# Kernel tuning notes

Hardware: AMD Instinct MI355X
Metric: run time of the kernel (lower is better)

The kernel has to match this reference:

```python
import jax, jax.numpy as jnp
import numpy as np

N = 40000      # nodes
E = 640000     # edges (before self-loops)
F_IN = 32      # num_node_features
H = 8          # n_heads
C = 16         # hidden_channels
G = 1000       # graphs in batch
M = 256        # MLP_neurons
NEG_SLOPE = 0.2


def setup_inputs() -> dict:
    key = jax.random.key(0)
    ks = jax.random.split(key, 24)
    d = {}
    d["x"] = jax.random.normal(ks[0], (N, F_IN), jnp.float32)
    d["edge_index"] = jax.random.randint(ks[1], (2, E), 0, N, dtype=jnp.int32)
    d["batch"] = jnp.sort(jax.random.randint(ks[2], (N,), 0, G, dtype=jnp.int32))
    dims = [F_IN, H * C, H * C]
    k = 3
    for i in range(3):
        fin = dims[i]
        s = 1.0 / np.sqrt(fin)
        d[f"W{i}"] = jax.random.normal(ks[k], (fin, H * C), jnp.float32) * s; k += 1
        d[f"b{i}"] = jnp.zeros((H * C,), jnp.float32)
        d[f"as{i}"] = jax.random.normal(ks[k], (H, C), jnp.float32) * (1.0 / np.sqrt(C)); k += 1
        d[f"ad{i}"] = jax.random.normal(ks[k], (H, C), jnp.float32) * (1.0 / np.sqrt(C)); k += 1
    d["fW0"] = jax.random.normal(ks[k], (H * C, M), jnp.float32) * (1.0 / np.sqrt(H * C)); k += 1
    d["fb0"] = jnp.zeros((M,), jnp.float32)
    d["fW1"] = jax.random.normal(ks[k], (M, M), jnp.float32) * (1.0 / np.sqrt(M)); k += 1
    d["fb1"] = jnp.zeros((M,), jnp.float32)
    d["oW"] = jax.random.normal(ks[k], (M, 2), jnp.float32) * (1.0 / np.sqrt(M)); k += 1
    d["ob"] = jnp.zeros((2,), jnp.float32)
    return d


def _gat_layer(x, W, b, a_src, a_dst, src, dst):
    # x: [N, Fin] -> h: [N, H, C]
    h = (x @ W).reshape(N, H, C)
    al_src = jnp.einsum('nhc,hc->nh', h, a_src)   # [N, H]
    al_dst = jnp.einsum('nhc,hc->nh', h, a_dst)   # [N, H]
    # edge-wise attention logits (gather), LeakyReLU
    e = jax.nn.leaky_relu(al_src[src] + al_dst[dst], NEG_SLOPE)  # [E', H]
    # softmax over incoming edges of each dst node
    emax = jax.ops.segment_max(e, dst, num_segments=N)           # [N, H]
    ex = jnp.exp(e - emax[dst])
    denom = jax.ops.segment_sum(ex, dst, num_segments=N)         # [N, H]
    alpha = ex / denom[dst]
    # weighted scatter-aggregation of source features
    out = jax.ops.segment_sum(alpha[:, :, None] * h[src], dst, num_segments=N)  # [N, H, C]
    return out.reshape(N, H * C) + b


def reference(x, edge_index, batch, W0, b0, as0, ad0, W1, b1, as1, ad1,
              W2, b2, as2, ad2, fW0, fb0, fW1, fb1, oW, ob):
    # PyG GATConv adds self-loops by default
    loops = jnp.arange(N, dtype=edge_index.dtype)
    src = jnp.concatenate([edge_index[0], loops])
    dst = jnp.concatenate([edge_index[1], loops])
    h = x
    for (W, b, a_s, a_d) in ((W0, b0, as0, ad0), (W1, b1, as1, ad1), (W2, b2, as2, ad2)):
        h = jax.nn.relu(_gat_layer(h, W, b, a_s, a_d, src, dst))
    # global mean pool per graph
    sums = jax.ops.segment_sum(h, batch, num_segments=G)                    # [G, H*C]
    cnts = jax.ops.segment_sum(jnp.ones((N,), h.dtype), batch, num_segments=G)
    g = sums / jnp.maximum(cnts, 1.0)[:, None]
    # MLP head (dropout is identity in eval mode)
    g = jax.nn.relu(g @ fW0 + fb0)
    g = jax.nn.relu(g @ fW1 + fb1)
    return g @ oW + ob
```

## Files before the change

kernel.cpp:

```cpp
#include <hip/hip_runtime.h>
#include <hip/hip_fp16.h>
#include <math.h>

#define NN 40000
#define EE 640000
#define EP 680000
#define FIN0 32
#define HC 128
#define GG 1000
#define MM 256
#define SCAN_BLOCKS ((NN + 255) / 256)
#define PROJ0_BLOCKS (NN / 64)
#define HIST_BLOCKS ((EP + 255) / 256)
#define PADH 136

typedef _Float16 f16x8 __attribute__((ext_vector_type(8)));
typedef float f32x4 __attribute__((ext_vector_type(4)));


__global__ __launch_bounds__(256) void prep_kernel(const float* __restrict__ X,
                                                   const float* __restrict__ W0,
                                                   const float* __restrict__ a_src,
                                                   const float* __restrict__ a_dst,
                                                   __half* __restrict__ H2,
                                                   float* __restrict__ als,
                                                   float* __restrict__ ald,
                                                   const int* __restrict__ ei,
                                                   int* __restrict__ deg,
                                                   int* __restrict__ rank,
                                                   const float* __restrict__ W1,
                                                   const float* __restrict__ W2,
                                                   __half* __restrict__ Wt1,
                                                   __half* __restrict__ Wt2) {
    int t = threadIdx.x;
    int b = blockIdx.x;
    if (b >= PROJ0_BLOCKS && b < PROJ0_BLOCKS + HIST_BLOCKS) {
        int idx = (b - PROJ0_BLOCKS) * 256 + t;
        if (idx < EP) {
            int d = (idx < EE) ? ei[EE + idx] : (idx - EE);
            rank[idx] = atomicAdd(&deg[d], 1);
        }
        return;
    }
    if (b >= PROJ0_BLOCKS + HIST_BLOCKS) {
        int l = b - (PROJ0_BLOCKS + HIST_BLOCKS);
        const float* Wsrc = (l == 0) ? W1 : W2;
        __half* Wd = (l == 0) ? Wt1 : Wt2;
#pragma unroll 8
        for (int r = 0; r < 64; r++) {
            int idx = r * 256 + t;
            int k = idx >> 7, c = idx & 127;
            Wd[c * 128 + k] = __float2half(Wsrc[idx]);
        }
        return;
    }
    __shared__ float xs[32][68];
    __shared__ float ws[32][128];
    int node0 = b * 64;
    int nt = t & 15;
    int ct = t >> 4;
    float acc[4][8];
#pragma unroll
    for (int i = 0; i < 4; i++)
#pragma unroll
        for (int j = 0; j < 8; j++) acc[i][j] = 0.f;
#pragma unroll
    for (int r = 0; r < 8; r++) {
        int idx = r * 256 + t;
        int n = idx >> 5, k = idx & 31;
        xs[k][n] = X[(node0 + n) * FIN0 + k];
    }
#pragma unroll
    for (int r = 0; r < 16; r++) {
        int idx = r * 256 + t;
        int k = idx >> 7, c = idx & 127;
        ws[k][c] = W0[k * 128 + c];
    }
    __syncthreads();
#pragma unroll
    for (int k = 0; k < 32; k++) {
        const float4 xv = *(const float4*)(&xs[k][4 * nt]);
        const float4 wa = *(const float4*)(&ws[k][8 * ct]);
        const float4 wb = *(const float4*)(&ws[k][8 * ct + 4]);
        float xr[4] = {xv.x, xv.y, xv.z, xv.w};
        float wr[8] = {wa.x, wa.y, wa.z, wa.w, wb.x, wb.y, wb.z, wb.w};
#pragma unroll
        for (int i = 0; i < 4; i++)
#pragma unroll
            for (int j = 0; j < 8; j++) acc[i][j] = fmaf(xr[i], wr[j], acc[i][j]);
    }
#pragma unroll
    for (int i = 0; i < 4; i++) {
        int n = node0 + 4 * nt + i;
        __half2 p0 = __floats2half2_rn(acc[i][0], acc[i][1]);
        __half2 p1 = __floats2half2_rn(acc[i][2], acc[i][3]);
        __half2 p2 = __floats2half2_rn(acc[i][4], acc[i][5]);
        __half2 p3 = __floats2half2_rn(acc[i][6], acc[i][7]);
        uint4 pk;
        pk.x = *(unsigned*)&p0; pk.y = *(unsigned*)&p1;
        pk.z = *(unsigned*)&p2; pk.w = *(unsigned*)&p3;
        *(uint4*)(&H2[(size_t)n * HC + 8 * ct]) = pk;
    }
    float sa[4] = {0.f, 0.f, 0.f, 0.f}, da[4] = {0.f, 0.f, 0.f, 0.f};
#pragma unroll
    for (int j = 0; j < 8; j++) {
        float av = a_src[ct * 8 + j];
        float dv = a_dst[ct * 8 + j];
#pragma unroll
        for (int i = 0; i < 4; i++) {
            sa[i] = fmaf(acc[i][j], av, sa[i]);
            da[i] = fmaf(acc[i][j], dv, da[i]);
        }
    }
#pragma unroll
    for (int i = 0; i < 4; i++) {
        sa[i] += __shfl_xor(sa[i], 16);
        da[i] += __shfl_xor(da[i], 16);
    }
    if ((ct & 1) == 0) {
        int head = ct >> 1;
#pragma unroll
        for (int i = 0; i < 4; i++) {
            int n = node0 + 4 * nt + i;
            als[n * 8 + head] = sa[i];
            ald[n * 8 + head] = da[i];
        }
    }
}


__global__ __launch_bounds__(256) void scan_partial(const int* __restrict__ deg,
                                                    int* __restrict__ part) {
    int b = blockIdx.x, t = threadIdx.x;
    int i = b * 256 + t;
    int v = (i < NN) ? deg[i] : 0;
#pragma unroll
    for (int d = 1; d < 64; d <<= 1) v += __shfl_xor(v, d);
    __shared__ int ws[4];
    if ((t & 63) == 0) ws[t >> 6] = v;
    __syncthreads();
    if (t == 0) part[b] = ws[0] + ws[1] + ws[2] + ws[3];
}

__global__ __launch_bounds__(256) void scan_final(const int* __restrict__ deg,
                                                  const int* __restrict__ part,
                                                  int* __restrict__ offs) {
    int b = blockIdx.x, t = threadIdx.x;
    __shared__ int sbase;
    if (t < 64) {
        int s = 0;
        for (int l = t; l < b; l += 64) s += part[l];
#pragma unroll
        for (int d = 1; d < 64; d <<= 1) s += __shfl_xor(s, d);
        if (t == 0) sbase = s;
    }
    int i = b * 256 + t;
    int v = (i < NN) ? deg[i] : 0;
    __shared__ int tmp[256];
    tmp[t] = v;
    __syncthreads();
    for (int st = 1; st < 256; st <<= 1) {
        int add = (t >= st) ? tmp[t - st] : 0;
        __syncthreads();
        tmp[t] += add;
        __syncthreads();
    }
    int excl = tmp[t] - v + sbase;
    if (i < NN) offs[i] = excl;
    if (i == NN - 1) offs[NN] = excl + v;
}

__global__ void scatter_kernel(const int* __restrict__ ei, const int* __restrict__ offs,
                               const int* __restrict__ rank, int* __restrict__ esrc) {
    int idx = blockIdx.x * 256 + threadIdx.x;
    if (idx >= EP) return;
    int s, d;
    if (idx < EE) { s = ei[idx]; d = ei[EE + idx]; } else { s = idx - EE; d = s; }
    esrc[offs[d] + rank[idx]] = s;
}


__global__ __launch_bounds__(256) void proj_mfma(const __half* __restrict__ Bin,
                                                 const __half* __restrict__ Wt,
                                                 const float* __restrict__ a_src,
                                                 const float* __restrict__ a_dst,
                                                 __half* __restrict__ H2,
                                                 float* __restrict__ als,
                                                 float* __restrict__ ald) {
    __shared__ __half As[64 * PADH];
    __shared__ __half Ws[128 * PADH];
    int t = threadIdx.x;
    int node0 = blockIdx.x * 64;
    {
        int n = t >> 2, kk = (t & 3) * 32;
        const uint4* src = (const uint4*)(&Bin[(size_t)(node0 + n) * 128 + kk]);
        uint4 v0 = src[0];
        uint4 v1 = src[1];
        uint4 v2 = src[2];
        uint4 v3 = src[3];
        uint4* dst = (uint4*)(&As[n * PADH + kk]);
        dst[0] = v0; dst[1] = v1; dst[2] = v2; dst[3] = v3;
    }
#pragma unroll
    for (int r = 0; r < 8; r++) {
        int idx = r * 256 + t;
        int c = idx >> 4;
        int kk = (idx & 15) * 8;
        uint4 v = *(const uint4*)(&Wt[c * 128 + kk]);
        *(uint4*)(&Ws[c * PADH + kk]) = v;
    }
    __syncthreads();
    int w = t >> 6, l = t & 63;
    int lr = l & 15, lg = l >> 4;
    f32x4 acc[8];
    f32x4 z4 = {0.f, 0.f, 0.f, 0.f};
#pragma unroll
    for (int n = 0; n < 8; n++) acc[n] = z4;
    const __half* arow = &As[(16 * w + lr) * PADH + lg * 8];
#pragma unroll
    for (int ks = 0; ks < 4; ks++) {
        f16x8 af = *(const f16x8*)(arow + 32 * ks);
#pragma unroll
        for (int n = 0; n < 8; n++) {
            f16x8 bf = *(const f16x8*)(&Ws[(16 * n + lr) * PADH + lg * 8 + 32 * ks]);
            acc[n] = __builtin_amdgcn_mfma_f32_16x16x32_f16(af, bf, acc[n], 0, 0, 0);
        }
    }
#pragma unroll
    for (int n = 0; n < 8; n++)
#pragma unroll
        for (int j = 0; j < 4; j++)
            As[(16 * w + lg * 4 + j) * PADH + 16 * n + lr] = __float2half(acc[n][j]);
    __syncthreads();
    {
        int n = t >> 2, kk = (t & 3) * 32;
        const uint4* src = (const uint4*)(&As[n * PADH + kk]);
        uint4 v0 = src[0];
        uint4 v1 = src[1];
        uint4 v2 = src[2];
        uint4 v3 = src[3];
        uint4* dst = (uint4*)(&H2[(size_t)(node0 + n) * 128 + kk]);
        dst[0] = v0; dst[1] = v1; dst[2] = v2; dst[3] = v3;
    }
    {
        int nt = t & 15, ct = t >> 4;
        float av[8], dv[8];
#pragma unroll
        for (int j = 0; j < 8; j++) { av[j] = a_src[ct * 8 + j]; dv[j] = a_dst[ct * 8 + j]; }
        float sa[4], da[4];
#pragma unroll
        for (int i = 0; i < 4; i++) {
            uint4 hv = *(const uint4*)(&As[(4 * nt + i) * PADH + 8 * ct]);
            __half2 h0 = *(__half2*)&hv.x;
            __half2 h1 = *(__half2*)&hv.y;
            __half2 h2 = *(__half2*)&hv.z;
            __half2 h3 = *(__half2*)&hv.w;
            float2 f0 = __half22float2(h0);
            float2 f1 = __half22float2(h1);
            float2 f2 = __half22float2(h2);
            float2 f3 = __half22float2(h3);
            sa[i] = f0.x * av[0] + f0.y * av[1] + f1.x * av[2] + f1.y * av[3] +
                    f2.x * av[4] + f2.y * av[5] + f3.x * av[6] + f3.y * av[7];
            da[i] = f0.x * dv[0] + f0.y * dv[1] + f1.x * dv[2] + f1.y * dv[3] +
                    f2.x * dv[4] + f2.y * dv[5] + f3.x * dv[6] + f3.y * dv[7];
        }
#pragma unroll
        for (int i = 0; i < 4; i++) {
            sa[i] += __shfl_xor(sa[i], 16);
            da[i] += __shfl_xor(da[i], 16);
        }
        if ((ct & 1) == 0) {
            int head = ct >> 1;
#pragma unroll
            for (int i = 0; i < 4; i++) {
                int n = node0 + 4 * nt + i;
                als[n * 8 + head] = sa[i];
                ald[n * 8 + head] = da[i];
            }
        }
    }
}


template <bool HALF_OUT>
__global__ __launch_bounds__(256) void agg_kernel(const __half* __restrict__ H2,
                                                  const float* __restrict__ als,
                                                  const float* __restrict__ ald,
                                                  const int* __restrict__ offs,
                                                  const int* __restrict__ esrc,
                                                  const float* __restrict__ bias,
                                                  float* __restrict__ OUT,
                                                  __half* __restrict__ OUT2) {
    int t = threadIdx.x;
    int n = blockIdx.x * 4 + (t >> 6);
    int t6 = t & 63;
    int c8 = t6 & 15;
    int slot = (t6 >> 4) & 3;
    int hd = c8 >> 1;
    int beg = offs[n], end = offs[n + 1];
    float ad = ald[n * 8 + hd];
    float acc[8] = {0.f, 0.f, 0.f, 0.f, 0.f, 0.f, 0.f, 0.f};
    float denom = 0.f;
    const float4* H4 = (const float4*)H2;

    int p = beg + slot;
    int s_cur = 0; float al_cur = 0.f;
    if (p < end) {
        s_cur = esrc[p];
        al_cur = als[s_cur * 8 + hd];
    }
#pragma unroll 2
    while (p < end) {
        int pn = p + 4;
        int s_nxt = 0;
        if (pn < end) s_nxt = esrc[pn];
        float x = al_cur + ad;
        x = (x > 0.f) ? x : 0.2f * x;
        float w = __expf(x);
        float4 r = H4[(size_t)s_cur * 16 + c8];
        float al_nxt = 0.f;
        if (pn < end) al_nxt = als[s_nxt * 8 + hd];
        __half2 h0 = *(__half2*)&r.x;
        __half2 h1 = *(__half2*)&r.y;
        __half2 h2 = *(__half2*)&r.z;
        __half2 h3 = *(__half2*)&r.w;
        float2 f0 = __half22float2(h0);
        float2 f1 = __half22float2(h1);
        float2 f2 = __half22float2(h2);
        float2 f3 = __half22float2(h3);
        acc[0] = fmaf(w, f0.x, acc[0]); acc[1] = fmaf(w, f0.y, acc[1]);
        acc[2] = fmaf(w, f1.x, acc[2]); acc[3] = fmaf(w, f1.y, acc[3]);
        acc[4] = fmaf(w, f2.x, acc[4]); acc[5] = fmaf(w, f2.y, acc[5]);
        acc[6] = fmaf(w, f3.x, acc[6]); acc[7] = fmaf(w, f3.y, acc[7]);
        denom += w;
        s_cur = s_nxt; al_cur = al_nxt;
        p = pn;
    }
#pragma unroll
    for (int j = 0; j < 8; j++) {
        acc[j] += __shfl_xor(acc[j], 16);
        acc[j] += __shfl_xor(acc[j], 32);
    }
    denom += __shfl_xor(denom, 16);
    denom += __shfl_xor(denom, 32);
    if (slot == 0 && t6 < 16) {
        float inv = 1.0f / denom;
        const float4 ba = ((const float4*)bias)[2 * c8];
        const float4 bb = ((const float4*)bias)[2 * c8 + 1];
        float o0 = fmaxf(fmaf(acc[0], inv, ba.x), 0.f);
        float o1 = fmaxf(fmaf(acc[1], inv, ba.y), 0.f);
        float o2 = fmaxf(fmaf(acc[2], inv, ba.z), 0.f);
        float o3 = fmaxf(fmaf(acc[3], inv, ba.w), 0.f);
        float o4 = fmaxf(fmaf(acc[4], inv, bb.x), 0.f);
        float o5 = fmaxf(fmaf(acc[5], inv, bb.y), 0.f);
        float o6 = fmaxf(fmaf(acc[6], inv, bb.z), 0.f);
        float o7 = fmaxf(fmaf(acc[7], inv, bb.w), 0.f);
        if (HALF_OUT) {
            __half2 q0 = __floats2half2_rn(o0, o1);
            __half2 q1 = __floats2half2_rn(o2, o3);
            __half2 q2 = __floats2half2_rn(o4, o5);
            __half2 q3 = __floats2half2_rn(o6, o7);
            uint4 pk;
            pk.x = *(unsigned*)&q0; pk.y = *(unsigned*)&q1;
            pk.z = *(unsigned*)&q2; pk.w = *(unsigned*)&q3;
            ((uint4*)OUT2)[(size_t)n * 16 + c8] = pk;
        } else {
            float4 v0, v1;
            v0.x = o0; v0.y = o1; v0.z = o2; v0.w = o3;
            v1.x = o4; v1.y = o5; v1.z = o6; v1.w = o7;
            ((float4*)OUT)[(size_t)n * 32 + 2 * c8]     = v0;
            ((float4*)OUT)[(size_t)n * 32 + 2 * c8 + 1] = v1;
        }
    }
}


__global__ __launch_bounds__(256) void mlp_fused(const float* __restrict__ B,
                                                 const int* __restrict__ batch,
                                                 const float* __restrict__ fW0,
                                                 const float* __restrict__ fb0,
                                                 const float* __restrict__ fW1,
                                                 const float* __restrict__ fb1,
                                                 const float* __restrict__ oW,
                                                 const float* __restrict__ ob,
                                                 float* __restrict__ out) {
    __shared__ int lo[3];
    __shared__ float rows[2][128];
    __shared__ float g1s[2][256];
    __shared__ float g2s[2][256];
    int t = threadIdx.x;
    int g0 = blockIdx.x * 2;
    if (t < 3) {
        int target = g0 + t;
        int a = 0, b = NN;
        while (a < b) { int mid = (a + b) >> 1; if (batch[mid] < target) a = mid + 1; else b = mid; }
        lo[t] = a;
    }
    __syncthreads();
    {
        int j = t >> 7, c = t & 127;
        int s0 = lo[j], s1 = lo[j + 1];
        float s = 0.f;
        float p0 = 0.f, p1 = 0.f, p2 = 0.f, p3 = 0.f;
        int n = s0;
        for (; n + 3 < s1; n += 4) {
            p0 += B[(size_t)n * 128 + c];
            p1 += B[(size_t)(n + 1) * 128 + c];
            p2 += B[(size_t)(n + 2) * 128 + c];
            p3 += B[(size_t)(n + 3) * 128 + c];
        }
        for (; n < s1; n++) s += B[(size_t)n * 128 + c];
        s += (p0 + p1) + (p2 + p3);
        rows[j][c] = s / fmaxf((float)(s1 - s0), 1.0f);
    }
    __syncthreads();
    float a0 = 0.f, a1 = 0.f;
#pragma unroll 8
    for (int k = 0; k < 128; k++) {
        float w = fW0[k * 256 + t];
        a0 = fmaf(rows[0][k], w, a0);
        a1 = fmaf(rows[1][k], w, a1);
    }
    float b0v = fb0[t];
    g1s[0][t] = fmaxf(a0 + b0v, 0.f);
    g1s[1][t] = fmaxf(a1 + b0v, 0.f);
    __syncthreads();
    a0 = 0.f; a1 = 0.f;
#pragma unroll 8
    for (int k = 0; k < 256; k++) {
        float w = fW1[k * 256 + t];
        a0 = fmaf(g1s[0][k], w, a0);
        a1 = fmaf(g1s[1][k], w, a1);
    }
    float b1v = fb1[t];
    g2s[0][t] = fmaxf(a0 + b1v, 0.f);
    g2s[1][t] = fmaxf(a1 + b1v, 0.f);
    __syncthreads();
    if (t < 64) {
        int jj = t >> 5, l = t & 31;
        float p0 = 0.f, p1 = 0.f;
#pragma unroll
        for (int k = l; k < 256; k += 32) {
            float v = g2s[jj][k];
            p0 = fmaf(v, oW[k * 2 + 0], p0);
            p1 = fmaf(v, oW[k * 2 + 1], p1);
        }
#pragma unroll
        for (int d = 1; d < 32; d <<= 1) {
            p0 += __shfl_xor(p0, d);
            p1 += __shfl_xor(p1, d);
        }
        if (l == 0) {
            out[(g0 + jj) * 2 + 0] = p0 + ob[0];
            out[(g0 + jj) * 2 + 1] = p1 + ob[1];
        }
    }
}


extern "C" void kernel_launch(void* const* d_in, const int* in_sizes, int n_in,
                              void* d_out, int out_size, void* d_ws, size_t ws_size,
                              hipStream_t stream) {
    const float* x    = (const float*)d_in[0];
    const int* ei     = (const int*)d_in[1];
    const int* batch  = (const int*)d_in[2];
    const float* W[3]   = {(const float*)d_in[3], (const float*)d_in[7],  (const float*)d_in[11]};
    const float* bs[3]  = {(const float*)d_in[4], (const float*)d_in[8],  (const float*)d_in[12]};
    const float* asr[3] = {(const float*)d_in[5], (const float*)d_in[9],  (const float*)d_in[13]};
    const float* adt[3] = {(const float*)d_in[6], (const float*)d_in[10], (const float*)d_in[14]};
    const float* fW0 = (const float*)d_in[15];
    const float* fb0 = (const float*)d_in[16];
    const float* fW1 = (const float*)d_in[17];
    const float* fb1 = (const float*)d_in[18];
    const float* oW  = (const float*)d_in[19];
    const float* ob  = (const float*)d_in[20];
    float* out = (float*)d_out;

    char* base = (char*)d_ws;
    size_t off = 0;
    auto alloc = [&](size_t bytes) -> void* {
        void* p = base + off;
        off += (bytes + 255) & ~(size_t)255;
        return p;
    };
    int* deg    = (int*)alloc((size_t)NN * 4);
    int* offs   = (int*)alloc((size_t)(NN + 1) * 4);
    int* part   = (int*)alloc((size_t)SCAN_BLOCKS * 4);
    int* rank   = (int*)alloc((size_t)EP * 4);
    int* esrc   = (int*)alloc((size_t)EP * 4);
    __half* H2  = (__half*)alloc((size_t)NN * HC * 2);
    float* B    = (float*)alloc((size_t)NN * HC * 4);
    __half* B2  = (__half*)alloc((size_t)NN * HC * 2);
    float* als  = (float*)alloc((size_t)NN * 8 * 4);
    float* ald  = (float*)alloc((size_t)NN * 8 * 4);
    __half* Wt1 = (__half*)alloc((size_t)HC * HC * 2);
    __half* Wt2 = (__half*)alloc((size_t)HC * HC * 2);

    hipMemsetAsync(deg, 0, (size_t)NN * 4, stream);

    prep_kernel<<<PROJ0_BLOCKS + HIST_BLOCKS + 2, 256, 0, stream>>>(
        x, W[0], asr[0], adt[0], H2, als, ald, ei, deg, rank, W[1], W[2], Wt1, Wt2);
    scan_partial<<<SCAN_BLOCKS, 256, 0, stream>>>(deg, part);
    scan_final<<<SCAN_BLOCKS, 256, 0, stream>>>(deg, part, offs);
    scatter_kernel<<<(EP + 255) / 256, 256, 0, stream>>>(ei, offs, rank, esrc);

    agg_kernel<true><<<NN / 4, 256, 0, stream>>>(H2, als, ald, offs, esrc, bs[0], nullptr, B2);
    proj_mfma<<<PROJ0_BLOCKS, 256, 0, stream>>>(B2, Wt1, asr[1], adt[1], H2, als, ald);
    agg_kernel<true><<<NN / 4, 256, 0, stream>>>(H2, als, ald, offs, esrc, bs[1], nullptr, B2);
    proj_mfma<<<PROJ0_BLOCKS, 256, 0, stream>>>(B2, Wt2, asr[2], adt[2], H2, als, ald);
    agg_kernel<false><<<NN / 4, 256, 0, stream>>>(H2, als, ald, offs, esrc, bs[2], B, nullptr);

    mlp_fused<<<GG / 2, 256, 0, stream>>>(B, batch, fW0, fb0, fW1, fb1, oW, ob, out);
}
```

Measured before the change: 295.4 us.

## Split agg channels across four blocks with 16 edge slots per node

The aggregation kernel now launches four times as many blocks. Each block handles a quarter of the 16 channel groups for four nodes, and a block-index swizzle keeps the four channel-quarters of the same nodes on nearby blocks. Within a wavefront, 16 edge slots run in parallel per node instead of 4, which shortens the serial per-edge loop for each node and raises parallelism and memory-level concurrency. In exchange, each edge's index, attention logit and exp are recomputed four times across blocks, and the cross-lane reduction needs more shuffles.

```diff
diff --git a/kernel.cpp b/kernel.cpp
--- a/kernel.cpp
+++ b/kernel.cpp
@@ -292,11 +292,15 @@
                                                   float* __restrict__ OUT,
                                                   __half* __restrict__ OUT2) {
     int t = threadIdx.x;
-    int n = blockIdx.x * 4 + (t >> 6);
+    int b = blockIdx.x;
+    int q = (b & 7) >> 1;
+    int g = ((b >> 3) << 1) | (b & 1);
+    int n = g * 4 + (t >> 6);
     int t6 = t & 63;
-    int c8 = t6 & 15;
-    int slot = (t6 >> 4) & 3;
-    int hd = c8 >> 1;
+    int c2 = t6 & 3;
+    int slot = t6 >> 2;
+    int cg = 4 * q + c2;
+    int hd = cg >> 1;
     int beg = offs[n], end = offs[n + 1];
     float ad = ald[n * 8 + hd];
     float acc[8] = {0.f, 0.f, 0.f, 0.f, 0.f, 0.f, 0.f, 0.f};
@@ -309,15 +313,14 @@
         s_cur = esrc[p];
         al_cur = als[s_cur * 8 + hd];
     }
-#pragma unroll 2
     while (p < end) {
-        int pn = p + 4;
+        int pn = p + 16;
         int s_nxt = 0;
         if (pn < end) s_nxt = esrc[pn];
         float x = al_cur + ad;
         x = (x > 0.f) ? x : 0.2f * x;
         float w = __expf(x);
-        float4 r = H4[(size_t)s_cur * 16 + c8];
+        float4 r = H4[(size_t)s_cur * 16 + cg];
         float al_nxt = 0.f;
         if (pn < end) al_nxt = als[s_nxt * 8 + hd];
         __half2 h0 = *(__half2*)&r.x;
@@ -338,15 +341,19 @@
     }
 #pragma unroll
     for (int j = 0; j < 8; j++) {
+        acc[j] += __shfl_xor(acc[j], 4);
+        acc[j] += __shfl_xor(acc[j], 8);
         acc[j] += __shfl_xor(acc[j], 16);
         acc[j] += __shfl_xor(acc[j], 32);
     }
+    denom += __shfl_xor(denom, 4);
+    denom += __shfl_xor(denom, 8);
     denom += __shfl_xor(denom, 16);
     denom += __shfl_xor(denom, 32);
-    if (slot == 0 && t6 < 16) {
+    if (slot == 0) {
         float inv = 1.0f / denom;
-        const float4 ba = ((const float4*)bias)[2 * c8];
-        const float4 bb = ((const float4*)bias)[2 * c8 + 1];
+        const float4 ba = ((const float4*)bias)[2 * cg];
+        const float4 bb = ((const float4*)bias)[2 * cg + 1];
         float o0 = fmaxf(fmaf(acc[0], inv, ba.x), 0.f);
         float o1 = fmaxf(fmaf(acc[1], inv, ba.y), 0.f);
         float o2 = fmaxf(fmaf(acc[2], inv, ba.z), 0.f);
@@ -363,13 +370,13 @@
             uint4 pk;
             pk.x = *(unsigned*)&q0; pk.y = *(unsigned*)&q1;
             pk.z = *(unsigned*)&q2; pk.w = *(unsigned*)&q3;
-            ((uint4*)OUT2)[(size_t)n * 16 + c8] = pk;
+            ((uint4*)OUT2)[(size_t)n * 16 + cg] = pk;
         } else {
             float4 v0, v1;
             v0.x = o0; v0.y = o1; v0.z = o2; v0.w = o3;
             v1.x = o4; v1.y = o5; v1.z = o6; v1.w = o7;
-            ((float4*)OUT)[(size_t)n * 32 + 2 * c8]     = v0;
-            ((float4*)OUT)[(size_t)n * 32 + 2 * c8 + 1] = v1;
+            ((float4*)OUT)[(size_t)n * 32 + 2 * cg]     = v0;
+            ((float4*)OUT)[(size_t)n * 32 + 2 * cg + 1] = v1;
         }
     }
 }
@@ -504,11 +511,11 @@
     scan_final<<<SCAN_BLOCKS, 256, 0, stream>>>(deg, part, offs);
     scatter_kernel<<<(EP + 255) / 256, 256, 0, stream>>>(ei, offs, rank, esrc);
 
-    agg_kernel<true><<<NN / 4, 256, 0, stream>>>(H2, als, ald, offs, esrc, bs[0], nullptr, B2);
+    agg_kernel<true><<<NN, 256, 0, stream>>>(H2, als, ald, offs, esrc, bs[0], nullptr, B2);
     proj_mfma<<<PROJ0_BLOCKS, 256, 0, stream>>>(B2, Wt1, asr[1], adt[1], H2, als, ald);
-    agg_kernel<true><<<NN / 4, 256, 0, stream>>>(H2, als, ald, offs, esrc, bs[1], nullptr, B2);
+    agg_kernel<true><<<NN, 256, 0, stream>>>(H2, als, ald, offs, esrc, bs[1], nullptr, B2);
     proj_mfma<<<PROJ0_BLOCKS, 256, 0, stream>>>(B2, Wt2, asr[2], adt[2], H2, als, ald);
-    agg_kernel<false><<<NN / 4, 256, 0, stream>>>(H2, als, ald, offs, esrc, bs[2], B, nullptr);
+    agg_kernel<false><<<NN, 256, 0, stream>>>(H2, als, ald, offs, esrc, bs[2], B, nullptr);
 
     mlp_fused<<<GG / 2, 256, 0, stream>>>(B, batch, fW0, fb0, fW1, fb1, oW, ob, out);
 }
```

Result: slower. 394.3 us (+33.5%).

## Replace atomic CSR build with two-pass LDS radix sort by destination

Applied to the files above, without the earlier changes.

Builds the destination-sorted edge list with a two-level radix sort instead of per-edge global atomics. Per-block shared-memory histograms over 256-node bins are scanned, then edges are scattered into bins as packed (dst,src) words, and a per-bin pass does a local counting sort to produce offsets and source indices. This drops the global degree atomics, the memset and the rank array, and gives more ordered writes. The cost is an extra pass over the edges and a reliance on 16-bit packing of node ids, which holds because N is below 65536.

```diff
diff --git a/kernel.cpp b/kernel.cpp
--- a/kernel.cpp
+++ b/kernel.cpp
@@ -9,9 +9,11 @@
 #define HC 128
 #define GG 1000
 #define MM 256
-#define SCAN_BLOCKS ((NN + 255) / 256)
 #define PROJ0_BLOCKS (NN / 64)
-#define HIST_BLOCKS ((EP + 255) / 256)
+#define NB 333
+#define NBIN 157
+#define HSIZE (NBIN * NB)
+#define SCAN2_BLOCKS ((HSIZE + 255) / 256)
 #define PADH 136
 
 typedef _Float16 f16x8 __attribute__((ext_vector_type(8)));
@@ -26,24 +28,33 @@
                                                    float* __restrict__ als,
                                                    float* __restrict__ ald,
                                                    const int* __restrict__ ei,
-                                                   int* __restrict__ deg,
-                                                   int* __restrict__ rank,
+                                                   int* __restrict__ hist,
                                                    const float* __restrict__ W1,
                                                    const float* __restrict__ W2,
                                                    __half* __restrict__ Wt1,
                                                    __half* __restrict__ Wt2) {
     int t = threadIdx.x;
     int b = blockIdx.x;
-    if (b >= PROJ0_BLOCKS && b < PROJ0_BLOCKS + HIST_BLOCKS) {
-        int idx = (b - PROJ0_BLOCKS) * 256 + t;
-        if (idx < EP) {
-            int d = (idx < EE) ? ei[EE + idx] : (idx - EE);
-            rank[idx] = atomicAdd(&deg[d], 1);
-        }
+    if (b >= PROJ0_BLOCKS && b < PROJ0_BLOCKS + NB) {
+        __shared__ int hb[NBIN];
+        int blk = b - PROJ0_BLOCKS;
+        for (int i = t; i < NBIN; i += 256) hb[i] = 0;
+        __syncthreads();
+        int base = blk * 2048 + t;
+#pragma unroll
+        for (int k = 0; k < 8; k++) {
+            int idx = base + k * 256;
+            if (idx < EP) {
+                int d = (idx < EE) ? ei[EE + idx] : (idx - EE);
+                atomicAdd(&hb[d >> 8], 1);
+            }
+        }
+        __syncthreads();
+        for (int i = t; i < NBIN; i += 256) hist[i * NB + blk] = hb[i];
         return;
     }
-    if (b >= PROJ0_BLOCKS + HIST_BLOCKS) {
-        int l = b - (PROJ0_BLOCKS + HIST_BLOCKS);
+    if (b >= PROJ0_BLOCKS + NB) {
+        int l = b - (PROJ0_BLOCKS + NB);
         const float* Wsrc = (l == 0) ? W1 : W2;
         __half* Wd = (l == 0) ? Wt1 : Wt2;
 #pragma unroll 8
@@ -129,11 +140,11 @@
 }
 
 
-__global__ __launch_bounds__(256) void scan_partial(const int* __restrict__ deg,
-                                                    int* __restrict__ part) {
+__global__ __launch_bounds__(256) void scan_partial2(const int* __restrict__ hist,
+                                                     int* __restrict__ part) {
     int b = blockIdx.x, t = threadIdx.x;
     int i = b * 256 + t;
-    int v = (i < NN) ? deg[i] : 0;
+    int v = (i < HSIZE) ? hist[i] : 0;
 #pragma unroll
     for (int d = 1; d < 64; d <<= 1) v += __shfl_xor(v, d);
     __shared__ int ws[4];
@@ -142,9 +153,9 @@
     if (t == 0) part[b] = ws[0] + ws[1] + ws[2] + ws[3];
 }
 
-__global__ __launch_bounds__(256) void scan_final(const int* __restrict__ deg,
-                                                  const int* __restrict__ part,
-                                                  int* __restrict__ offs) {
+__global__ __launch_bounds__(256) void scan_final2(const int* __restrict__ hist,
+                                                   const int* __restrict__ part,
+                                                   int* __restrict__ base) {
     int b = blockIdx.x, t = threadIdx.x;
     __shared__ int sbase;
     if (t < 64) {
@@ -155,7 +166,7 @@
         if (t == 0) sbase = s;
     }
     int i = b * 256 + t;
-    int v = (i < NN) ? deg[i] : 0;
+    int v = (i < HSIZE) ? hist[i] : 0;
     __shared__ int tmp[256];
     tmp[t] = v;
     __syncthreads();
@@ -166,17 +177,71 @@
         __syncthreads();
     }
     int excl = tmp[t] - v + sbase;
-    if (i < NN) offs[i] = excl;
-    if (i == NN - 1) offs[NN] = excl + v;
-}
-
-__global__ void scatter_kernel(const int* __restrict__ ei, const int* __restrict__ offs,
-                               const int* __restrict__ rank, int* __restrict__ esrc) {
-    int idx = blockIdx.x * 256 + threadIdx.x;
-    if (idx >= EP) return;
-    int s, d;
-    if (idx < EE) { s = ei[idx]; d = ei[EE + idx]; } else { s = idx - EE; d = s; }
-    esrc[offs[d] + rank[idx]] = s;
+    if (i < HSIZE) base[i] = excl;
+}
+
+
+__global__ __launch_bounds__(256) void radix_c1(const int* __restrict__ ei,
+                                                const int* __restrict__ base,
+                                                unsigned* __restrict__ tmp) {
+    __shared__ int lbase[NBIN];
+    __shared__ int lcnt[NBIN];
+    int t = threadIdx.x, blk = blockIdx.x;
+    for (int i = t; i < NBIN; i += 256) { lbase[i] = base[i * NB + blk]; lcnt[i] = 0; }
+    __syncthreads();
+    int start = blk * 2048 + t;
+#pragma unroll
+    for (int k = 0; k < 8; k++) {
+        int idx = start + k * 256;
+        if (idx < EP) {
+            int s, d;
+            if (idx < EE) { s = ei[idx]; d = ei[EE + idx]; } else { s = idx - EE; d = s; }
+            int bin = d >> 8;
+            int r = atomicAdd(&lcnt[bin], 1);
+            tmp[lbase[bin] + r] = ((unsigned)d << 16) | (unsigned)s;
+        }
+    }
+}
+
+
+__global__ __launch_bounds__(256) void radix_p2(const unsigned* __restrict__ tmp,
+                                                const int* __restrict__ base,
+                                                int* __restrict__ esrc,
+                                                int* __restrict__ offs) {
+    __shared__ int cnt[256];
+    __shared__ int sc[256];
+    int t = threadIdx.x, k = blockIdx.x;
+    int bb = base[k * NB];
+    int be = (k == NBIN - 1) ? EP : base[(k + 1) * NB];
+    cnt[t] = 0;
+    __syncthreads();
+    for (int e = bb + t; e < be; e += 256) {
+        unsigned v = tmp[e];
+        atomicAdd(&cnt[(v >> 16) & 255], 1);
+    }
+    __syncthreads();
+    int myc = cnt[t];
+    sc[t] = myc;
+    __syncthreads();
+    for (int st = 1; st < 256; st <<= 1) {
+        int add = (t >= st) ? sc[t - st] : 0;
+        __syncthreads();
+        sc[t] += add;
+        __syncthreads();
+    }
+    int ex = sc[t] - myc;
+    int d = k * 256 + t;
+    if (d < NN) offs[d] = bb + ex;
+    if (k == NBIN - 1 && t == 0) offs[NN] = EP;
+    __syncthreads();
+    cnt[t] = ex;
+    __syncthreads();
+    for (int e = bb + t; e < be; e += 256) {
+        unsigned v = tmp[e];
+        int d0 = (v >> 16) & 255;
+        int r = atomicAdd(&cnt[d0], 1);
+        esrc[bb + r] = (int)(v & 0xFFFFu);
+    }
 }
 
 
@@ -476,18 +541,19 @@
     const float* ob  = (const float*)d_in[20];
     float* out = (float*)d_out;
 
-    char* base = (char*)d_ws;
+    char* base_ws = (char*)d_ws;
     size_t off = 0;
     auto alloc = [&](size_t bytes) -> void* {
-        void* p = base + off;
+        void* p = base_ws + off;
         off += (bytes + 255) & ~(size_t)255;
         return p;
     };
-    int* deg    = (int*)alloc((size_t)NN * 4);
-    int* offs   = (int*)alloc((size_t)(NN + 1) * 4);
-    int* part   = (int*)alloc((size_t)SCAN_BLOCKS * 4);
-    int* rank   = (int*)alloc((size_t)EP * 4);
-    int* esrc   = (int*)alloc((size_t)EP * 4);
+    int* hist     = (int*)alloc((size_t)HSIZE * 4);
+    int* sbase    = (int*)alloc((size_t)HSIZE * 4);
+    int* part     = (int*)alloc((size_t)SCAN2_BLOCKS * 4);
+    unsigned* tmp = (unsigned*)alloc((size_t)EP * 4);
+    int* offs     = (int*)alloc((size_t)(NN + 1) * 4);
+    int* esrc     = (int*)alloc((size_t)EP * 4);
     __half* H2  = (__half*)alloc((size_t)NN * HC * 2);
     float* B    = (float*)alloc((size_t)NN * HC * 4);
     __half* B2  = (__half*)alloc((size_t)NN * HC * 2);
@@ -496,13 +562,12 @@
     __half* Wt1 = (__half*)alloc((size_t)HC * HC * 2);
     __half* Wt2 = (__half*)alloc((size_t)HC * HC * 2);
 
-    hipMemsetAsync(deg, 0, (size_t)NN * 4, stream);
-
-    prep_kernel<<<PROJ0_BLOCKS + HIST_BLOCKS + 2, 256, 0, stream>>>(
-        x, W[0], asr[0], adt[0], H2, als, ald, ei, deg, rank, W[1], W[2], Wt1, Wt2);
-    scan_partial<<<SCAN_BLOCKS, 256, 0, stream>>>(deg, part);
-    scan_final<<<SCAN_BLOCKS, 256, 0, stream>>>(deg, part, offs);
-    scatter_kernel<<<(EP + 255) / 256, 256, 0, stream>>>(ei, offs, rank, esrc);
+    prep_kernel<<<PROJ0_BLOCKS + NB + 2, 256, 0, stream>>>(
+        x, W[0], asr[0], adt[0], H2, als, ald, ei, hist, W[1], W[2], Wt1, Wt2);
+    scan_partial2<<<SCAN2_BLOCKS, 256, 0, stream>>>(hist, part);
+    scan_final2<<<SCAN2_BLOCKS, 256, 0, stream>>>(hist, part, sbase);
+    radix_c1<<<NB, 256, 0, stream>>>(ei, sbase, tmp);
+    radix_p2<<<NBIN, 256, 0, stream>>>(tmp, sbase, esrc, offs);
 
     agg_kernel<true><<<NN / 4, 256, 0, stream>>>(H2, als, ald, offs, esrc, bs[0], nullptr, B2);
     proj_mfma<<<PROJ0_BLOCKS, 256, 0, stream>>>(B2, Wt1, asr[1], adt[1], H2, als, ald);
```

Result: faster. 288.2 us (median of 2 runs) (-2.5%).
